# Performance work log

Hardware: AMD Instinct MI355X
Metric: run time of the kernel (lower is better)

Reference implementation:

```python
import jax, jax.numpy as jnp
import numpy as np

N = 100000          # nodes
E = 1600000         # edges
IN, H, E1, E2, K = 256, 128, 128, 128, 3


def setup_inputs() -> dict:
    key = jax.random.key(0)
    ks = jax.random.split(key, 8)
    s = 0.02
    return {
        "x": jax.random.normal(ks[0], (N, IN), dtype=jnp.float32),
        "edge_index": jax.random.randint(ks[1], (2, E), 0, N),
        "edge_weight": jax.random.uniform(ks[2], (E,), dtype=jnp.float32),
        "W1": jax.random.normal(ks[3], (IN, H), dtype=jnp.float32) * s,
        "b1": jnp.zeros((H,), jnp.float32),
        "cheb1_W": jax.random.normal(ks[4], (K, H, E1), dtype=jnp.float32) * s,
        "cheb1_b": jnp.zeros((E1,), jnp.float32),
        "cheb2_W": jax.random.normal(ks[5], (K, E1, E2), dtype=jnp.float32) * s,
        "cheb2_b": jnp.zeros((E2,), jnp.float32),
        "W2": jax.random.normal(ks[6], (E2, 2), dtype=jnp.float32) * s,
        "b2": jnp.zeros((2,), jnp.float32),
    }


def _cheb_conv(x, row, col, wn, Ws, b):
    """PyG ChebConv with sym normalization, lambda_max=2.
    Scaled Laplacian L_hat = L_sym - I = -D^{-1/2} A D^{-1/2} (zero diagonal),
    so L_hat @ v is a single gather/scale/scatter over edges.
    Tx_0 = x; Tx_1 = L_hat x; Tx_k = 2 L_hat Tx_{k-1} - Tx_{k-2}.
    """
    n = x.shape[0]

    def Lx(v):
        return jax.ops.segment_sum(-wn[:, None] * v[col], row, num_segments=n)

    Tx0 = x
    out = Tx0 @ Ws[0]
    Tx1 = Lx(Tx0)
    out = out + Tx1 @ Ws[1]
    for k in range(2, Ws.shape[0]):
        Tx2 = 2.0 * Lx(Tx1) - Tx0
        out = out + Tx2 @ Ws[k]
        Tx0, Tx1 = Tx1, Tx2
    return out + b


def reference(x, edge_index, edge_weight, W1, b1, cheb1_W, cheb1_b,
              cheb2_W, cheb2_b, W2, b2):
    row, col = edge_index[0], edge_index[1]
    n = x.shape[0]
    # symmetric normalization of edge weights (shared by both convs)
    deg = jax.ops.segment_sum(edge_weight, row, num_segments=n)
    safe = jnp.where(deg > 0, deg, 1.0)
    dinv = jnp.where(deg > 0, jax.lax.rsqrt(safe), 0.0)
    wn = dinv[row] * edge_weight * dinv[col]

    # dropout is identity in eval mode
    h = jax.nn.relu(x @ W1 + b1)
    h = jax.nn.relu(_cheb_conv(h, row, col, wn, cheb1_W, cheb1_b))
    h = jax.nn.relu(_cheb_conv(h, row, col, wn, cheb2_W, cheb2_b))
    logits = h @ W2 + b2
    return jax.nn.softmax(logits, axis=1)
```

## Files before the change

### kernel.cpp

```cpp
#include <hip/hip_runtime.h>
#include <hip/hip_bf16.h>
#include <stdint.h>

typedef __bf16 bf16_t;
typedef __bf16 bf16x8 __attribute__((ext_vector_type(8)));
typedef float f32x4 __attribute__((ext_vector_type(4)));
typedef float f32x2 __attribute__((ext_vector_type(2)));
typedef float floatv4 __attribute__((ext_vector_type(4)));

static __device__ __forceinline__ void gload16(const void* g, void* l){
  __builtin_amdgcn_global_load_lds((const __attribute__((address_space(1))) void*)g,
                                   (__attribute__((address_space(3))) void*)l, 16, 0, 0);
}
static __device__ __forceinline__ void acc4_fp8(float* a, unsigned w, float wt){
  f32x2 lo, hi;
  unsigned wh = w >> 16;
  asm("v_cvt_pk_f32_fp8 %0, %1" : "=v"(lo) : "v"(w));
  asm("v_cvt_pk_f32_fp8 %0, %1" : "=v"(hi) : "v"(wh));
  a[0] += wt*lo[0]; a[1] += wt*lo[1]; a[2] += wt*hi[0]; a[3] += wt*hi[1];
}
static __device__ __forceinline__ void dec4_fp8(float* d, unsigned w){
  f32x2 lo, hi;
  unsigned wh = w >> 16;
  asm("v_cvt_pk_f32_fp8 %0, %1" : "=v"(lo) : "v"(w));
  asm("v_cvt_pk_f32_fp8 %0, %1" : "=v"(hi) : "v"(wh));
  d[0] = lo[0]; d[1] = lo[1]; d[2] = hi[0]; d[3] = hi[1];
}
static __device__ __forceinline__ unsigned cvt2fp8(float a, float b){
  unsigned r;
  asm("v_cvt_pk_fp8_f32 %0, %1, %2" : "=v"(r) : "v"(a), "v"(b));
  return r & 0xffffu;
}
static __device__ __forceinline__ uint8_t cvt1fp8(float a){
  unsigned r;
  asm("v_cvt_pk_fp8_f32 %0, %1, %1" : "=v"(r) : "v"(a));
  return (uint8_t)r;
}
static __device__ __forceinline__ unsigned packEdge(int col, float w_pos){
  unsigned b = __float_as_uint(w_pos) + 0x8000u;
  return ((b >> 16) << 17) | (unsigned)col;
}
static __device__ __forceinline__ float edgeWpos(unsigned u){
  return __uint_as_float((u >> 17) << 16);
}
static __device__ __forceinline__ float edgeWneg(unsigned u){
  return __uint_as_float(0x80000000u | ((u >> 17) << 16));
}

constexpr int NN = 100000;
constexpr int NE = 1600000;
constexpr int NB_G  = (NN + 127)/128;
constexpr int NBIN = (NN + 127)/128;
constexpr int EPB  = 4096;
constexpr int NBB  = (NE + EPB - 1)/EPB;
constexpr int MAXBE = 3072;
constexpr int NB_TW8 = (2*3*128*128)/256;
constexpr int NB_TW1 = (2*128*128)/256;

__global__ __launch_bounds__(256) void k_binA_tw(const int* __restrict__ row,
                                                 int* __restrict__ bincnt,
                                                 int* __restrict__ blockbase,
                                                 const float* __restrict__ W1,
                                                 bf16_t* __restrict__ Wt1){
  __shared__ int h[NBIN];
  const int tid = threadIdx.x;
  if (blockIdx.x >= NBB){
    int idx = (blockIdx.x - NBB)*256 + tid;
    int c = idx >> 14, r = (idx >> 7) & 127, j = idx & 127;
    Wt1[(c << 14) + (j << 7) + r] = (bf16_t)W1[idx];
    return;
  }
  for (int b = tid; b < NBIN; b += 256) h[b] = 0;
  __syncthreads();
  int base = blockIdx.x * EPB;
  for (int k = 0; k < EPB; k += 256){
    int i = base + k + tid;
    if (i < NE) atomicAdd(&h[row[i] >> 7], 1);
  }
  __syncthreads();
  for (int b = tid; b < NBIN; b += 256){
    int c = h[b];
    blockbase[blockIdx.x * NBIN + b] = c ? atomicAdd(&bincnt[b], c) : 0;
  }
}

__global__ __launch_bounds__(256) void k_scanbins(const int* __restrict__ bincnt,
                                                  int* __restrict__ binptr,
                                                  int* __restrict__ rowptr){
  __shared__ int s[256];
  int t = threadIdx.x;
  int b0 = t*4;
  int c[4]; int tot = 0;
  #pragma unroll
  for (int j = 0; j < 4; ++j){
    int b = b0 + j;
    c[j] = (b < NBIN) ? bincnt[b] : 0;
    tot += c[j];
  }
  s[t] = tot;
  __syncthreads();
  for (int off = 1; off < 256; off <<= 1){
    int v = (t >= off) ? s[t - off] : 0;
    __syncthreads();
    s[t] += v;
    __syncthreads();
  }
  int ex = s[t] - tot;
  #pragma unroll
  for (int j = 0; j < 4; ++j){
    int b = b0 + j;
    if (b < NBIN) binptr[b] = ex;
    ex += c[j];
  }
  if (t == 255){ binptr[NBIN] = ex; rowptr[NN] = ex; }
}

__global__ __launch_bounds__(256) void k_binC(const int2* __restrict__ temp,
                                              const int* __restrict__ binptr,
                                              unsigned* __restrict__ ec,
                                              int* __restrict__ rowptr,
                                              float* __restrict__ dinv, int n){
  __shared__ int2 sbuf[MAXBE];
  __shared__ int cnt[128];
  __shared__ int scan[128];
  __shared__ int estart[128];
  const int b = blockIdx.x;
  const int e0 = binptr[b];
  int nb = binptr[b+1] - e0; if (nb > MAXBE) nb = MAXBE;
  const int t = threadIdx.x;
  if (t < 128) cnt[t] = 0;
  __syncthreads();
  for (int k = t; k < nb; k += 256)
    atomicAdd(&cnt[(temp[e0+k].x >> 17) & 127], 1);
  __syncthreads();
  if (t < 128) scan[t] = cnt[t];
  __syncthreads();
  for (int off = 1; off < 128; off <<= 1){
    int v = (t < 128 && t >= off) ? scan[t - off] : 0;
    __syncthreads();
    if (t < 128) scan[t] += v;
    __syncthreads();
  }
  if (t < 128){ estart[t] = scan[t] - cnt[t]; cnt[t] = 0; }
  __syncthreads();
  for (int k = t; k < nb; k += 256){
    int2 q = temp[e0+k];
    int rl = (q.x >> 17) & 127;
    int rank = atomicAdd(&cnt[rl], 1);
    sbuf[estart[rl] + rank] = q;
  }
  __syncthreads();
  for (int k = t; k < nb; k += 256){
    int2 q = sbuf[k];
    ec[e0 + k] = packEdge(q.x & 0x1FFFF, __int_as_float(q.y));
  }
  if (t < 128){
    int gid = b*128 + t;
    if (gid < n){
      rowptr[gid] = e0 + estart[t];
      float s = 0.f;
      int s0 = estart[t], c = cnt[t];
      for (int j = 0; j < c; ++j) s += __int_as_float(sbuf[s0+j].y);
      dinv[gid] = (s > 0.f) ? rsqrtf(s) : 0.f;
    }
  }
}

__global__ __launch_bounds__(256) void k_gemm1_fused(
    const float* __restrict__ x, const bf16_t* __restrict__ Wt, const float* __restrict__ bias,
    uint8_t* __restrict__ out8, int M,
    const int* __restrict__ row, const int* __restrict__ col, const float* __restrict__ w,
    const int* __restrict__ binptr, const int* __restrict__ blockbase, int2* __restrict__ temp,
    const float* __restrict__ c1W, const float* __restrict__ c2W,
    uint8_t* __restrict__ W8c1, uint8_t* __restrict__ W8c2)
{
  __shared__ uint8_t lds[2][16384];
  __shared__ int hB[NBIN];
  const int tid = threadIdx.x;

  if (blockIdx.x >= NB_G + NBB){
    int base = (blockIdx.x - NB_G - NBB)*256 + tid;
    int m = base / 49152;
    int local = base - m*49152;
    const float* src = m ? c2W : c1W;
    uint8_t* dst = m ? W8c2 : W8c1;
    int c = local >> 14, r = (local >> 7) & 127, j = local & 127;
    dst[(c << 14) + (j << 7) + r] = cvt1fp8(src[local]);
    return;
  }
  if (blockIdx.x >= NB_G){
    int bb = blockIdx.x - NB_G;
    for (int b = tid; b < NBIN; b += 256) hB[b] = 0;
    __syncthreads();
    int base = bb * EPB;
    for (int k = 0; k < EPB; k += 256){
      int i = base + k + tid;
      if (i < NE){
        int r = row[i];
        int b = r >> 7;
        int rank = atomicAdd(&hB[b], 1);
        int pos = binptr[b] + blockbase[bb * NBIN + b] + rank;
        temp[pos] = make_int2(col[i] | ((r & 127) << 17), __float_as_int(w[i]));
      }
    }
    return;
  }

  const int wave = tid >> 6, lane = tid & 63;
  const int wm = wave >> 1, wn = wave & 1;
  const int l15 = lane & 15, lq = lane >> 4;
  const int blockRow = blockIdx.x * 128;
  const int strow = tid >> 3;
  const int scell = tid & 7;

  f32x4 acc[4][4];
  #pragma unroll
  for (int a = 0; a < 4; ++a)
    #pragma unroll
    for (int b = 0; b < 4; ++b) acc[a][b] = f32x4{0.f,0.f,0.f,0.f};

  #pragma unroll
  for (int j = 0; j < 4; ++j){
    int r = j*32 + strow;
    int gr = blockRow + r; if (gr > M-1) gr = M-1;
    gload16((const char*)x + (size_t)gr*1024 + ((scell ^ (r&7)) << 4),
            &lds[0][j*4096 + tid*16]);
  }

  #pragma unroll
  for (int s = 0; s < 8; ++s){
    if (s < 7){
      #pragma unroll
      for (int j = 0; j < 4; ++j){
        int r = j*32 + strow;
        int gr = blockRow + r; if (gr > M-1) gr = M-1;
        gload16((const char*)x + (size_t)gr*1024 + (s+1)*128 + ((scell ^ (r&7)) << 4),
                &lds[(s+1)&1][j*4096 + tid*16]);
      }
    }
    __syncthreads();
    const uint8_t* buf = lds[s&1];
    bf16x8 af[4], bfr[4];
    #pragma unroll
    for (int fm = 0; fm < 4; ++fm){
      int r = wm*64 + fm*16 + l15;
      floatv4 v0 = *(const floatv4*)(buf + r*128 + (((lq*2    ) ^ (r&7)) << 4));
      floatv4 v1 = *(const floatv4*)(buf + r*128 + (((lq*2 + 1) ^ (r&7)) << 4));
      bf16x8 t;
      t[0]=(bf16_t)v0[0]; t[1]=(bf16_t)v0[1]; t[2]=(bf16_t)v0[2]; t[3]=(bf16_t)v0[3];
      t[4]=(bf16_t)v1[0]; t[5]=(bf16_t)v1[1]; t[6]=(bf16_t)v1[2]; t[7]=(bf16_t)v1[3];
      af[fm] = t;
    }
    #pragma unroll
    for (int fn = 0; fn < 4; ++fn)
      bfr[fn] = *(const bf16x8*)(Wt + ((size_t)(((s>>2) << 7) + wn*64 + fn*16 + l15) << 7) + (s&3)*32 + lq*8);
    #pragma unroll
    for (int fm = 0; fm < 4; ++fm)
      #pragma unroll
      for (int fn = 0; fn < 4; ++fn)
        acc[fm][fn] = __builtin_amdgcn_mfma_f32_16x16x32_bf16(af[fm], bfr[fn], acc[fm][fn], 0, 0, 0);
    __syncthreads();
  }
  #pragma unroll
  for (int fm = 0; fm < 4; ++fm){
    #pragma unroll
    for (int j = 0; j < 4; ++j){
      int growo = blockRow + wm*64 + fm*16 + lq*4 + j;
      if (growo < M){
        #pragma unroll
        for (int fn = 0; fn < 4; ++fn){
          int c = wn*64 + fn*16 + l15;
          float v = fmaxf(acc[fm][fn][j] + bias[c], 0.f);
          out8[((size_t)growo << 7) + c] = cvt1fp8(v);
        }
      }
    }
  }
}

__global__ __launch_bounds__(256) void k_gemm8(
    const uint8_t* __restrict__ a0, const uint8_t* __restrict__ a1, const uint8_t* __restrict__ a2,
    const uint8_t* __restrict__ Wt8, const float* __restrict__ bias,
    uint8_t* __restrict__ out8,
    const float* __restrict__ W2h, const float* __restrict__ b2h, float* __restrict__ outh,
    int M)
{
  __shared__ uint8_t lds[2][8192];
  __shared__ float logits[128][2][2];
  const int tid = threadIdx.x;
  const int wave = tid >> 6, lane = tid & 63;
  const int wm = wave >> 1, wn = wave & 1;
  const int l15 = lane & 15, lq = lane >> 4;
  const int blockRow = blockIdx.x * 128;

  f32x4 acc[4][4];
  #pragma unroll
  for (int a = 0; a < 4; ++a)
    #pragma unroll
    for (int b = 0; b < 4; ++b) acc[a][b] = f32x4{0.f,0.f,0.f,0.f};

  #pragma unroll
  for (int j = 0; j < 2; ++j){
    int flat = j*256 + tid;
    int r = flat >> 2, cell = flat & 3;
    int gr = blockRow + r; if (gr > M-1) gr = M-1;
    gload16(a0 + (size_t)gr*128 + ((cell ^ ((r>>1)&3)) << 4), &lds[0][flat << 4]);
  }

  #pragma unroll
  for (int s = 0; s < 6; ++s){
    if (s < 5){
      const int sn = s + 1;
      const uint8_t* srcn = (sn>>1) == 0 ? a0 : ((sn>>1) == 1 ? a1 : a2);
      #pragma unroll
      for (int j = 0; j < 2; ++j){
        int flat = j*256 + tid;
        int r = flat >> 2, cell = flat & 3;
        int gr = blockRow + r; if (gr > M-1) gr = M-1;
        gload16(srcn + (size_t)gr*128 + (sn&1)*64 + ((cell ^ ((r>>1)&3)) << 4),
                &lds[sn&1][flat << 4]);
      }
    }
    __syncthreads();
    const uint8_t* buf = lds[s&1];
    #pragma unroll
    for (int kk32 = 0; kk32 < 2; ++kk32){
      long af[4], bfr[4];
      #pragma unroll
      for (int fm = 0; fm < 4; ++fm){
        int r = wm*64 + fm*16 + l15;
        int cell = kk32*2 + (lq >> 1);
        af[fm] = *(const long*)(buf + r*64 + ((cell ^ ((r>>1)&3)) << 4) + (lq & 1)*8);
      }
      #pragma unroll
      for (int fn = 0; fn < 4; ++fn)
        bfr[fn] = *(const long*)(Wt8 + ((size_t)(((s>>1) << 7) + wn*64 + fn*16 + l15) << 7)
                                 + (s&1)*64 + kk32*32 + lq*8);
      #pragma unroll
      for (int fm = 0; fm < 4; ++fm)
        #pragma unroll
        for (int fn = 0; fn < 4; ++fn)
          acc[fm][fn] = __builtin_amdgcn_mfma_f32_16x16x32_fp8_fp8(af[fm], bfr[fn], acc[fm][fn], 0, 0, 0);
    }
    __syncthreads();
  }

  if (outh){
    float w2l[8];
    #pragma unroll
    for (int fn = 0; fn < 4; ++fn){
      int c = wn*64 + fn*16 + l15;
      w2l[fn*2]   = W2h[c*2];
      w2l[fn*2+1] = W2h[c*2+1];
    }
    #pragma unroll
    for (int fm = 0; fm < 4; ++fm){
      #pragma unroll
      for (int j = 0; j < 4; ++j){
        int r = wm*64 + fm*16 + lq*4 + j;
        float p0 = 0.f, p1 = 0.f;
        #pragma unroll
        for (int fn = 0; fn < 4; ++fn){
          float v = fmaxf(acc[fm][fn][j] + bias[wn*64 + fn*16 + l15], 0.f);
          p0 += v*w2l[fn*2];
          p1 += v*w2l[fn*2+1];
        }
        #pragma unroll
        for (int m = 1; m < 16; m <<= 1){
          p0 += __shfl_xor(p0, m, 64);
          p1 += __shfl_xor(p1, m, 64);
        }
        if (l15 == 0){
          logits[r][wn][0] = p0;
          logits[r][wn][1] = p1;
        }
      }
    }
    __syncthreads();
    if (tid < 128){
      int node = blockRow + tid;
      if (node < M){
        float l0 = logits[tid][0][0] + logits[tid][1][0] + b2h[0];
        float l1 = logits[tid][0][1] + logits[tid][1][1] + b2h[1];
        float mx = fmaxf(l0, l1);
        float e0 = __expf(l0 - mx), e1 = __expf(l1 - mx);
        float inv = 1.f / (e0 + e1);
        *(float2*)(outh + (size_t)node*2) = make_float2(e0*inv, e1*inv);
      }
    }
  } else {
    #pragma unroll
    for (int fm = 0; fm < 4; ++fm){
      #pragma unroll
      for (int j = 0; j < 4; ++j){
        int growo = blockRow + wm*64 + fm*16 + lq*4 + j;
        if (growo < M){
          #pragma unroll
          for (int fn = 0; fn < 4; ++fn){
            int c = wn*64 + fn*16 + l15;
            float v = fmaxf(acc[fm][fn][j] + bias[c], 0.f);
            out8[((size_t)growo << 7) + c] = cvt1fp8(v);
          }
        }
      }
    }
  }
}

__global__ __launch_bounds__(256) void k_spmm8n(
    const int* __restrict__ rowptr, unsigned* __restrict__ ec,
    const float* __restrict__ dinv,
    const uint8_t* __restrict__ V8, uint8_t* __restrict__ out8, int n)
{
  const int lane = threadIdx.x & 63;
  const int wave = threadIdx.x >> 6;
  const int g = lane >> 4;
  const int s = lane & 15;
  const int node = blockIdx.x*16 + wave*4 + g;
  if (node >= n) return;

  int e = rowptr[node];
  const int e1 = rowptr[node+1];
  const int fb = s << 3;
  const float dr = dinv[node];

  float acc[8] = {0.f,0.f,0.f,0.f,0.f,0.f,0.f,0.f};

  for (; e + 4 <= e1; e += 4){
    unsigned u0 = ec[e], u1 = ec[e+1], u2 = ec[e+2], u3 = ec[e+3];
    int c0 = u0 & 0x1FFFF, c1 = u1 & 0x1FFFF, c2 = u2 & 0x1FFFF, c3 = u3 & 0x1FFFF;
    uint2 p0 = *(const uint2*)(V8 + (((size_t)c0) << 7) + fb);
    uint2 p1 = *(const uint2*)(V8 + (((size_t)c1) << 7) + fb);
    uint2 p2 = *(const uint2*)(V8 + (((size_t)c2) << 7) + fb);
    uint2 p3 = *(const uint2*)(V8 + (((size_t)c3) << 7) + fb);
    float wn0 = dr * edgeWpos(u0) * dinv[c0];
    float wn1 = dr * edgeWpos(u1) * dinv[c1];
    float wn2 = dr * edgeWpos(u2) * dinv[c2];
    float wn3 = dr * edgeWpos(u3) * dinv[c3];
    if (s == 0){
      ec[e]   = packEdge(c0, wn0);
      ec[e+1] = packEdge(c1, wn1);
      ec[e+2] = packEdge(c2, wn2);
      ec[e+3] = packEdge(c3, wn3);
    }
    acc4_fp8(acc, p0.x, -wn0); acc4_fp8(acc+4, p0.y, -wn0);
    acc4_fp8(acc, p1.x, -wn1); acc4_fp8(acc+4, p1.y, -wn1);
    acc4_fp8(acc, p2.x, -wn2); acc4_fp8(acc+4, p2.y, -wn2);
    acc4_fp8(acc, p3.x, -wn3); acc4_fp8(acc+4, p3.y, -wn3);
  }
  for (; e < e1; ++e){
    unsigned u = ec[e];
    int c = u & 0x1FFFF;
    uint2 p = *(const uint2*)(V8 + (((size_t)c) << 7) + fb);
    float wn = dr * edgeWpos(u) * dinv[c];
    if (s == 0) ec[e] = packEdge(c, wn);
    acc4_fp8(acc, p.x, -wn); acc4_fp8(acc+4, p.y, -wn);
  }

  uint2 o8;
  o8.x = cvt2fp8(acc[0], acc[1]) | (cvt2fp8(acc[2], acc[3]) << 16);
  o8.y = cvt2fp8(acc[4], acc[5]) | (cvt2fp8(acc[6], acc[7]) << 16);
  *(uint2*)(out8 + (((size_t)node) << 7) + fb) = o8;
}

__global__ __launch_bounds__(256) void k_spmm8(
    const int* __restrict__ rowptr, const unsigned* __restrict__ ec,
    const uint8_t* __restrict__ V8, const uint8_t* __restrict__ sub8, float alpha,
    uint8_t* __restrict__ out8, int n)
{
  const int lane = threadIdx.x & 63;
  const int wave = threadIdx.x >> 6;
  const int g = lane >> 4;
  const int s = lane & 15;
  const int node = blockIdx.x*16 + wave*4 + g;
  if (node >= n) return;

  int e = rowptr[node];
  const int e1 = rowptr[node+1];
  const int fb = s << 3;

  float acc[8] = {0.f,0.f,0.f,0.f,0.f,0.f,0.f,0.f};

  for (; e + 8 <= e1; e += 8){
    unsigned u0 = ec[e],   u1 = ec[e+1], u2 = ec[e+2], u3 = ec[e+3];
    unsigned u4 = ec[e+4], u5 = ec[e+5], u6 = ec[e+6], u7 = ec[e+7];
    uint2 p0 = *(const uint2*)(V8 + (((size_t)(u0 & 0x1FFFF)) << 7) + fb);
    uint2 p1 = *(const uint2*)(V8 + (((size_t)(u1 & 0x1FFFF)) << 7) + fb);
    uint2 p2 = *(const uint2*)(V8 + (((size_t)(u2 & 0x1FFFF)) << 7) + fb);
    uint2 p3 = *(const uint2*)(V8 + (((size_t)(u3 & 0x1FFFF)) << 7) + fb);
    uint2 p4 = *(const uint2*)(V8 + (((size_t)(u4 & 0x1FFFF)) << 7) + fb);
    uint2 p5 = *(const uint2*)(V8 + (((size_t)(u5 & 0x1FFFF)) << 7) + fb);
    uint2 p6 = *(const uint2*)(V8 + (((size_t)(u6 & 0x1FFFF)) << 7) + fb);
    uint2 p7 = *(const uint2*)(V8 + (((size_t)(u7 & 0x1FFFF)) << 7) + fb);
    float w0 = edgeWneg(u0), w1 = edgeWneg(u1), w2 = edgeWneg(u2), w3 = edgeWneg(u3);
    float w4 = edgeWneg(u4), w5 = edgeWneg(u5), w6 = edgeWneg(u6), w7 = edgeWneg(u7);
    acc4_fp8(acc,   p0.x, w0); acc4_fp8(acc+4, p0.y, w0);
    acc4_fp8(acc,   p1.x, w1); acc4_fp8(acc+4, p1.y, w1);
    acc4_fp8(acc,   p2.x, w2); acc4_fp8(acc+4, p2.y, w2);
    acc4_fp8(acc,   p3.x, w3); acc4_fp8(acc+4, p3.y, w3);
    acc4_fp8(acc,   p4.x, w4); acc4_fp8(acc+4, p4.y, w4);
    acc4_fp8(acc,   p5.x, w5); acc4_fp8(acc+4, p5.y, w5);
    acc4_fp8(acc,   p6.x, w6); acc4_fp8(acc+4, p6.y, w6);
    acc4_fp8(acc,   p7.x, w7); acc4_fp8(acc+4, p7.y, w7);
  }
  for (; e + 4 <= e1; e += 4){
    unsigned u0 = ec[e], u1 = ec[e+1], u2 = ec[e+2], u3 = ec[e+3];
    uint2 p0 = *(const uint2*)(V8 + (((size_t)(u0 & 0x1FFFF)) << 7) + fb);
    uint2 p1 = *(const uint2*)(V8 + (((size_t)(u1 & 0x1FFFF)) << 7) + fb);
    uint2 p2 = *(const uint2*)(V8 + (((size_t)(u2 & 0x1FFFF)) << 7) + fb);
    uint2 p3 = *(const uint2*)(V8 + (((size_t)(u3 & 0x1FFFF)) << 7) + fb);
    float w0 = edgeWneg(u0), w1 = edgeWneg(u1), w2 = edgeWneg(u2), w3 = edgeWneg(u3);
    acc4_fp8(acc,   p0.x, w0); acc4_fp8(acc+4, p0.y, w0);
    acc4_fp8(acc,   p1.x, w1); acc4_fp8(acc+4, p1.y, w1);
    acc4_fp8(acc,   p2.x, w2); acc4_fp8(acc+4, p2.y, w2);
    acc4_fp8(acc,   p3.x, w3); acc4_fp8(acc+4, p3.y, w3);
  }
  for (; e < e1; ++e){
    unsigned u = ec[e];
    uint2 p = *(const uint2*)(V8 + (((size_t)(u & 0x1FFFF)) << 7) + fb);
    float w = edgeWneg(u);
    acc4_fp8(acc, p.x, w); acc4_fp8(acc+4, p.y, w);
  }

  float r[8];
  #pragma unroll
  for (int i = 0; i < 8; ++i) r[i] = alpha*acc[i];
  if (sub8){
    uint2 sv = *(const uint2*)(sub8 + (((size_t)node) << 7) + fb);
    float sd[8];
    dec4_fp8(sd,     sv.x);
    dec4_fp8(sd + 4, sv.y);
    #pragma unroll
    for (int i = 0; i < 8; ++i) r[i] -= sd[i];
  }
  uint2 o8;
  o8.x = cvt2fp8(r[0], r[1]) | (cvt2fp8(r[2], r[3]) << 16);
  o8.y = cvt2fp8(r[4], r[5]) | (cvt2fp8(r[6], r[7]) << 16);
  *(uint2*)(out8 + (((size_t)node) << 7) + fb) = o8;
}


extern "C" void kernel_launch(void* const* d_in, const int* in_sizes, int n_in,
                              void* d_out, int out_size, void* d_ws, size_t ws_size,
                              hipStream_t stream)
{
  const float* x   = (const float*)d_in[0];
  const int*   ei  = (const int*)d_in[1];
  const float* ew  = (const float*)d_in[2];
  const float* W1  = (const float*)d_in[3];
  const float* b1  = (const float*)d_in[4];
  const float* c1W = (const float*)d_in[5];
  const float* c1b = (const float*)d_in[6];
  const float* c2W = (const float*)d_in[7];
  const float* c2b = (const float*)d_in[8];
  const float* W2  = (const float*)d_in[9];
  const float* b2  = (const float*)d_in[10];
  float* out = (float*)d_out;

  const int n = NN, e = NE;
  const int* row = ei;
  const int* col = ei + e;

  char* ws = (char*)d_ws;
  size_t off = 0;
  auto carve = [&](size_t bytes)->void*{
    void* p = ws + off;
    off += (bytes + 255) & ~(size_t)255;
    return p;
  };
  uint8_t* q8a = (uint8_t*)carve((size_t)n*128);
  uint8_t* B8  = (uint8_t*)carve((size_t)n*128);
  uint8_t* C8  = (uint8_t*)carve((size_t)n*128);
  uint8_t* D8  = (uint8_t*)carve((size_t)n*128);
  float*  dinv = (float*)carve((size_t)n*4);
  int*    rowptr = (int*)carve((size_t)(n+1)*4);
  unsigned* ec = (unsigned*)carve((size_t)e*4);
  int*    bincnt = (int*)carve((size_t)NBIN*4);
  int*    binptr = (int*)carve((size_t)(NBIN+1)*4);
  int*    blockbase = (int*)carve((size_t)NBB*NBIN*4);
  bf16_t*  Wt1  = (bf16_t*)carve(2*128*128*2);
  uint8_t* W8c1 = (uint8_t*)carve(3*128*128);
  uint8_t* W8c2 = (uint8_t*)carve(3*128*128);
  int2* temp = (int2*)D8;
  (void)ws_size; (void)in_sizes; (void)n_in; (void)out_size;

  const int NB_S = (n + 15)/16;

  hipMemsetAsync(bincnt, 0, (size_t)NBIN*4, stream);
  k_binA_tw<<<NBB + NB_TW1,256,0,stream>>>(row, bincnt, blockbase, W1, Wt1);
  k_scanbins<<<1,256,0,stream>>>(bincnt, binptr, rowptr);
  k_gemm1_fused<<<NB_G + NBB + NB_TW8,256,0,stream>>>(
      x, Wt1, b1, q8a, n, row, col, ew, binptr, blockbase, temp, c1W, c2W, W8c1, W8c2);
  k_binC<<<NBIN,256,0,stream>>>(temp, binptr, ec, rowptr, dinv, n);

  k_spmm8n<<<NB_S,256,0,stream>>>(rowptr, ec, dinv, q8a, B8, n);
  k_spmm8<<<NB_S,256,0,stream>>>(rowptr, ec, B8, q8a, 2.f, C8, n);
  k_gemm8<<<NB_G,256,0,stream>>>(q8a, B8, C8, W8c1, c1b, D8, nullptr, nullptr, nullptr, n);
  k_spmm8<<<NB_S,256,0,stream>>>(rowptr, ec, D8, nullptr, 1.f, B8, n);
  k_spmm8<<<NB_S,256,0,stream>>>(rowptr, ec, B8, D8, 2.f, C8, n);
  k_gemm8<<<NB_G,256,0,stream>>>(D8, B8, C8, W8c2, c2b, nullptr, W2, b2, out, n);
}
```

Baseline: 295.2 us.

## Fold Chebyshev recurrence into weights and stage binned edges in LDS

Rewrites the Chebyshev combination algebraically. Since Tx2 = 2*L*Tx1 - Tx0, the output x0*W0 + Tx1*W1 + Tx2*W2 equals x0*(W0-W2) + Tx1*W1 + (L*Tx1)*(2*W2), so the fp8 weights are pre-transformed and the SpMM no longer loads or subtracts the Tx0 term or applies alpha. Separately, the edge-binning blocks now count per bin, scan in LDS, stage the edges in shared memory, then write each bin's run contiguously to global memory instead of scattering one edge at a time. This cuts a feature read per node in two SpMMs and aims for more coalesced writes, at the cost of different fp8 rounding (the weight difference and doubling are quantized) and extra syncs in the binning blocks.

```diff
diff --git a/kernel.cpp b/kernel.cpp
--- a/kernel.cpp
+++ b/kernel.cpp
@@ -18,13 +18,6 @@
   asm("v_cvt_pk_f32_fp8 %0, %1" : "=v"(lo) : "v"(w));
   asm("v_cvt_pk_f32_fp8 %0, %1" : "=v"(hi) : "v"(wh));
   a[0] += wt*lo[0]; a[1] += wt*lo[1]; a[2] += wt*hi[0]; a[3] += wt*hi[1];
-}
-static __device__ __forceinline__ void dec4_fp8(float* d, unsigned w){
-  f32x2 lo, hi;
-  unsigned wh = w >> 16;
-  asm("v_cvt_pk_f32_fp8 %0, %1" : "=v"(lo) : "v"(w));
-  asm("v_cvt_pk_f32_fp8 %0, %1" : "=v"(hi) : "v"(wh));
-  d[0] = lo[0]; d[1] = lo[1]; d[2] = hi[0]; d[3] = hi[1];
 }
 static __device__ __forceinline__ unsigned cvt2fp8(float a, float b){
   unsigned r;
@@ -174,8 +167,7 @@
     const float* __restrict__ c1W, const float* __restrict__ c2W,
     uint8_t* __restrict__ W8c1, uint8_t* __restrict__ W8c2)
 {
-  __shared__ uint8_t lds[2][16384];
-  __shared__ int hB[NBIN];
+  __shared__ char smem[40964];
   const int tid = threadIdx.x;
 
   if (blockIdx.x >= NB_G + NBB){
@@ -185,27 +177,73 @@
     const float* src = m ? c2W : c1W;
     uint8_t* dst = m ? W8c2 : W8c1;
     int c = local >> 14, r = (local >> 7) & 127, j = local & 127;
-    dst[(c << 14) + (j << 7) + r] = cvt1fp8(src[local]);
+    float v = src[local];
+    if (c == 0) v -= src[2*16384 + local];
+    if (c == 2) v *= 2.f;
+    dst[(c << 14) + (j << 7) + r] = cvt1fp8(v);
     return;
   }
   if (blockIdx.x >= NB_G){
-    int bb = blockIdx.x - NB_G;
-    for (int b = tid; b < NBIN; b += 256) hB[b] = 0;
-    __syncthreads();
-    int base = bb * EPB;
+    int2* stage = (int2*)smem;
+    int*  base_ = (int*)(smem + 32768);
+    int*  rank_ = (int*)(smem + 35904);
+    int*  saux  = (int*)(smem + 39040);
+    const int bb = blockIdx.x - NB_G;
+    const int ebase = bb * EPB;
+    for (int b = tid; b < NBIN; b += 256){ base_[b] = 0; rank_[b] = 0; }
+    __syncthreads();
     for (int k = 0; k < EPB; k += 256){
-      int i = base + k + tid;
+      int i = ebase + k + tid;
+      if (i < NE) atomicAdd(&base_[row[i] >> 7], 1);
+    }
+    __syncthreads();
+    int b0 = tid*4;
+    int c[4]; int tot = 0;
+    #pragma unroll
+    for (int j = 0; j < 4; ++j){
+      int b = b0 + j;
+      c[j] = (b < NBIN) ? base_[b] : 0;
+      tot += c[j];
+    }
+    saux[tid] = tot;
+    __syncthreads();
+    for (int off = 1; off < 256; off <<= 1){
+      int v = (tid >= off) ? saux[tid - off] : 0;
+      __syncthreads();
+      saux[tid] += v;
+      __syncthreads();
+    }
+    int ex = saux[tid] - tot;
+    #pragma unroll
+    for (int j = 0; j < 4; ++j){
+      int b = b0 + j;
+      if (b < NBIN) base_[b] = ex;
+      ex += c[j];
+    }
+    if (tid == 255) base_[NBIN] = ex;
+    __syncthreads();
+    for (int k = 0; k < EPB; k += 256){
+      int i = ebase + k + tid;
       if (i < NE){
         int r = row[i];
         int b = r >> 7;
-        int rank = atomicAdd(&hB[b], 1);
-        int pos = binptr[b] + blockbase[bb * NBIN + b] + rank;
-        temp[pos] = make_int2(col[i] | ((r & 127) << 17), __float_as_int(w[i]));
+        int rk = atomicAdd(&rank_[b], 1);
+        stage[base_[b] + rk] = make_int2(col[i] | ((r & 127) << 17), __float_as_int(w[i]));
+      }
+    }
+    __syncthreads();
+    for (int b = tid; b < NBIN; b += 256){
+      int s0 = base_[b];
+      int cnt = base_[b+1] - s0;
+      if (cnt){
+        int dst = binptr[b] + blockbase[bb * NBIN + b];
+        for (int r = 0; r < cnt; ++r) temp[dst + r] = stage[s0 + r];
       }
     }
     return;
   }
 
+  uint8_t (*lds)[16384] = (uint8_t(*)[16384])smem;
   const int wave = tid >> 6, lane = tid & 63;
   const int wm = wave >> 1, wn = wave & 1;
   const int l15 = lane & 15, lq = lane >> 4;
@@ -465,8 +503,7 @@
 
 __global__ __launch_bounds__(256) void k_spmm8(
     const int* __restrict__ rowptr, const unsigned* __restrict__ ec,
-    const uint8_t* __restrict__ V8, const uint8_t* __restrict__ sub8, float alpha,
-    uint8_t* __restrict__ out8, int n)
+    const uint8_t* __restrict__ V8, uint8_t* __restrict__ out8, int n)
 {
   const int lane = threadIdx.x & 63;
   const int wave = threadIdx.x >> 6;
@@ -522,20 +559,9 @@
     acc4_fp8(acc, p.x, w); acc4_fp8(acc+4, p.y, w);
   }
 
-  float r[8];
-  #pragma unroll
-  for (int i = 0; i < 8; ++i) r[i] = alpha*acc[i];
-  if (sub8){
-    uint2 sv = *(const uint2*)(sub8 + (((size_t)node) << 7) + fb);
-    float sd[8];
-    dec4_fp8(sd,     sv.x);
-    dec4_fp8(sd + 4, sv.y);
-    #pragma unroll
-    for (int i = 0; i < 8; ++i) r[i] -= sd[i];
-  }
   uint2 o8;
-  o8.x = cvt2fp8(r[0], r[1]) | (cvt2fp8(r[2], r[3]) << 16);
-  o8.y = cvt2fp8(r[4], r[5]) | (cvt2fp8(r[6], r[7]) << 16);
+  o8.x = cvt2fp8(acc[0], acc[1]) | (cvt2fp8(acc[2], acc[3]) << 16);
+  o8.y = cvt2fp8(acc[4], acc[5]) | (cvt2fp8(acc[6], acc[7]) << 16);
   *(uint2*)(out8 + (((size_t)node) << 7) + fb) = o8;
 }
 
@@ -594,9 +620,9 @@
   k_binC<<<NBIN,256,0,stream>>>(temp, binptr, ec, rowptr, dinv, n);
 
   k_spmm8n<<<NB_S,256,0,stream>>>(rowptr, ec, dinv, q8a, B8, n);
-  k_spmm8<<<NB_S,256,0,stream>>>(rowptr, ec, B8, q8a, 2.f, C8, n);
+  k_spmm8<<<NB_S,256,0,stream>>>(rowptr, ec, B8, C8, n);
   k_gemm8<<<NB_G,256,0,stream>>>(q8a, B8, C8, W8c1, c1b, D8, nullptr, nullptr, nullptr, n);
-  k_spmm8<<<NB_S,256,0,stream>>>(rowptr, ec, D8, nullptr, 1.f, B8, n);
-  k_spmm8<<<NB_S,256,0,stream>>>(rowptr, ec, B8, D8, 2.f, C8, n);
+  k_spmm8<<<NB_S,256,0,stream>>>(rowptr, ec, D8, B8, n);
+  k_spmm8<<<NB_S,256,0,stream>>>(rowptr, ec, B8, C8, n);
   k_gemm8<<<NB_G,256,0,stream>>>(D8, B8, C8, W8c2, c2b, nullptr, W2, b2, out, n);
 }
```

Result: no change. 292.8 us (median of 2 runs) (-0.8%).
